# Kernel optimization log

Measured on AMD Instinct MI355X. Metric: run time of the kernel, lower is better.

Reference implementation:

```python
import jax, jax.numpy as jnp
import numpy as np


def setup_inputs() -> dict:
    key = jax.random.key(0)
    k1, k2 = jax.random.split(key)
    B, Fin, N = 8, 64, 4096
    Fout, K = 64, 20
    x = jax.random.normal(k1, (B, Fin, N), dtype=jnp.float32)
    W = jax.random.normal(k2, (Fout, 2 * Fin), dtype=jnp.float32) * (1.0 / np.sqrt(2 * Fin))
    b = jnp.zeros((Fout,), dtype=jnp.float32)
    return {"x": x, "W": W, "b": b, "k": K}


def reference(x, W, b, k):
    # x: [B, Fin, N]; W: [Fout, 2Fin] (1x1 conv weight); b: [Fout]
    B, Fin, N = x.shape
    xt = jnp.swapaxes(x, 1, 2)                      # [B, N, Fin]
    sq = jnp.sum(xt * xt, axis=2)                   # [B, N]
    # pairwise squared distances: ||xi||^2 - 2 xi.xj + ||xj||^2
    dist = -2.0 * jnp.einsum('bnf,bmf->bnm', xt, xt) + sq[:, :, None] + sq[:, None, :]
    # ascending sort, drop self (index 0), keep k nearest neighbors
    idx = jnp.argsort(dist, axis=2)[:, :, 1:k + 1]  # [B, N, k] int
    # gather neighbor features per batch
    nbr = jax.vmap(lambda pts, i: pts[i])(xt, idx)  # [B, N, k, Fin]
    central = xt[:, :, None, :]                     # [B, N, 1, Fin]
    ee = jnp.concatenate(
        [jnp.broadcast_to(central, (B, N, k, Fin)), nbr - central], axis=-1
    )                                               # [B, N, k, 2Fin]
    # 1x1 conv == dense over channel dim, then bias, then max over k
    h = jnp.einsum('bnkf,of->bnko', ee, W) + b      # [B, N, k, Fout]
    out = jnp.max(h, axis=2)                        # [B, N, Fout]
    return jnp.swapaxes(out, 1, 2)                  # [B, Fout, N]
```

## Files before the change

### kernel.cpp

```cpp
#include <hip/hip_runtime.h>
#include <hip/hip_bf16.h>
#include <float.h>


#define BB 8
#define FF 64
#define NN 4096
#define KK 20
#define CAP 64
#define SS 4
#define PAD 1.0f

typedef unsigned short ushort_t;
typedef unsigned long long u64;
typedef __attribute__((ext_vector_type(8))) _Float16 half8;
typedef __attribute__((ext_vector_type(4))) float floatx4;
typedef __attribute__((ext_vector_type(2))) float floatx2;
typedef __attribute__((ext_vector_type(2))) unsigned short ushortx2;
typedef __attribute__((ext_vector_type(4))) unsigned int uintx4;

__device__ __forceinline__ size_t plidx16(int b, int n, int k) {
  return ((size_t)b * 256 + (n >> 4)) * 1024 + (size_t)(k >> 3) * 128 + (size_t)(n & 15) * 8 + (k & 7);
}

__global__ void __launch_bounds__(256) prep_kernel(
    const float* __restrict__ x, const float* __restrict__ W,
    float* __restrict__ sq, float* __restrict__ Q,
    ushort_t* __restrict__ ph, ushort_t* __restrict__ pm)
{
  __shared__ float xs[64][65];
  __shared__ float w2[64][65];
  int t = threadIdx.x;
  int b = blockIdx.x >> 6;
  int n0 = (blockIdx.x & 63) << 6;
  const float* xb = x + (size_t)b * FF * NN;

  int nl = t & 63, fq = t >> 6;
  #pragma unroll
  for (int i = 0; i < 16; ++i) {
    int f = fq + i * 4;
    xs[f][nl] = xb[(size_t)f * NN + n0 + nl];
  }
  #pragma unroll
  for (int i = 0; i < 16; ++i) {
    int id = i * 256 + t;
    int o = id >> 6, f = id & 63;
    w2[o][f] = W[o * 128 + 64 + f];
  }
  __syncthreads();

  if (t < 64) {
    float s = 0.f;
    #pragma unroll
    for (int f = 0; f < FF; ++f) { float v = xs[f][t]; s += v * v; }
    sq[b * NN + n0 + t] = s;
  }
  int o = t & 63, g = t >> 6;
  for (int i = 0; i < 16; ++i) {
    int r = g + i * 4;
    int n = n0 + r;
    float acc = 0.f;
    #pragma unroll
    for (int f = 0; f < FF; ++f) acc += w2[o][f] * xs[f][r];
    Q[((size_t)b * NN + n) * FF + o] = acc;

    float v = xs[o][r] * 1.41421356237309515f;
    _Float16 hh = (_Float16)v;
    float hf = (float)hh;
    _Float16 mm = (_Float16)((v - hf) * 4096.0f);
    size_t pb = plidx16(b, n, o);
    ph[pb] = __builtin_bit_cast(unsigned short, hh);
    pm[pb] = __builtin_bit_cast(unsigned short, mm);
  }
}

__device__ __forceinline__ void bitonic32f(float& v0, float& v1, int l15)
{
  #pragma unroll
  for (int k = 2; k <= 32; k <<= 1) {
    #pragma unroll
    for (int j = k >> 1; j >= 1; j >>= 1) {
      bool dirup = ((2 * l15) & k) == 0;
      if (j >= 2) {
        int lj = j >> 1;
        float p0 = __shfl_xor(v0, lj, 16);
        float p1 = __shfl_xor(v1, lj, 16);
        bool lower = (l15 & lj) == 0;
        bool keepmin = (dirup == lower);
        v0 = keepmin ? fminf(v0, p0) : fmaxf(v0, p0);
        v1 = keepmin ? fminf(v1, p1) : fmaxf(v1, p1);
      } else {
        float lo = fminf(v0, v1), hi = fmaxf(v0, v1);
        v0 = dirup ? lo : hi;
        v1 = dirup ? hi : lo;
      }
    }
  }
}

__device__ __forceinline__ void bitonic64k(u64& v0, u64& v1, int l31)
{
  #pragma unroll
  for (int k = 2; k <= 64; k <<= 1) {
    #pragma unroll
    for (int j = k >> 1; j >= 1; j >>= 1) {
      bool dirup = ((2 * l31) & k) == 0;
      if (j >= 2) {
        int lj = j >> 1;
        u64 p0 = __shfl_xor(v0, lj, 32);
        u64 p1 = __shfl_xor(v1, lj, 32);
        bool lower = (l31 & lj) == 0;
        bool keepmin = (dirup == lower);
        u64 a0 = v0 < p0 ? v0 : p0, b0 = v0 < p0 ? p0 : v0;
        u64 a1 = v1 < p1 ? v1 : p1, b1 = v1 < p1 ? p1 : v1;
        v0 = keepmin ? a0 : b0;
        v1 = keepmin ? a1 : b1;
      } else {
        u64 lo = v0 < v1 ? v0 : v1, hi = v0 < v1 ? v1 : v0;
        v0 = dirup ? lo : hi;
        v1 = dirup ? hi : lo;
      }
    }
  }
}

__device__ __forceinline__ u64 mkkey(float d, unsigned short idx)
{
  unsigned ub = __float_as_uint(d);
  unsigned mono = ub ^ (0x80000000u | (unsigned)((int)ub >> 31));
  return ((u64)mono << 16) | idx;
}

__global__ void __launch_bounds__(256) knn_kernel(
    const ushort_t* __restrict__ ph, const ushort_t* __restrict__ pm,
    const float* __restrict__ sq, u64* __restrict__ keys2)
{
  __shared__ float    bufd[4][16][CAP];
  __shared__ ushort_t bufi[4][16][CAP];
  __shared__ int scnt[4][16];

  const int t = threadIdx.x;
  const int lane = t & 63;
  const int l15 = lane & 15;
  const int q = lane >> 4;
  const int wv = t >> 6;
  const int blk = blockIdx.x;
  const int slice = blk & 3;
  const int g = (blk >> 2) & 63;
  const int b = blk >> 8;
  const int n0w = (g * 4 + wv) * 16;

  const float* __restrict__ sqb = sq + (size_t)b * NN;
  const float MS = 2.44140625e-4f;
  const int laneoff = q * 128 + l15 * 8;

  const bool hasdiag = ((n0w >> 10) == slice);
  const int dmc = (n0w & 1023) >> 5;

  half8 Ah[2], Am[2];
  {
    size_t abase = ((size_t)b * 256 + (n0w >> 4)) * 1024 + laneoff;
    #pragma unroll
    for (int s = 0; s < 2; ++s) {
      Ah[s] = *(const half8*)(ph + abase + s * 512);
      Am[s] = *(const half8*)(pm + abase + s * 512);
      uintx4 uh = __builtin_bit_cast(uintx4, Ah[s]); uh ^= 0x80008000u;
      uintx4 um = __builtin_bit_cast(uintx4, Am[s]); um ^= 0x80008000u;
      Ah[s] = __builtin_bit_cast(half8, uh);
      Am[s] = __builtin_bit_cast(half8, um);
    }
  }

  float m1[4], m2[4];
  #pragma unroll
  for (int r = 0; r < 4; ++r) { m1[r] = FLT_MAX; m2[r] = FLT_MAX; }

  for (int mc = 0; mc < 32; ++mc) {
    const int m0 = slice * 1024 + mc * 32;
    size_t mbase = ((size_t)b * 256 + (m0 >> 4)) * 1024 + laneoff;
    float sv0 = sqb[m0 + l15];
    float sv1 = sqb[m0 + 16 + l15];
    floatx4 a1[2];
    #pragma unroll
    for (int e = 0; e < 4; ++e) { a1[0][e] = sv0; a1[1][e] = sv1; }
    #pragma unroll
    for (int ti = 0; ti < 2; ++ti) {
      #pragma unroll
      for (int s = 0; s < 2; ++s) {
        half8 Bh = *(const half8*)(ph + mbase + ti * 1024 + s * 512);
        a1[ti] = __builtin_amdgcn_mfma_f32_16x16x32_f16(Ah[s], Bh, a1[ti], 0, 0, 0);
      }
    }
    if (hasdiag && mc == dmc) {
      #pragma unroll
      for (int ti = 0; ti < 2; ++ti) {
        int mcol = m0 + 16 * ti + l15;
        #pragma unroll
        for (int r = 0; r < 4; ++r)
          if (mcol == n0w + 4 * q + r) a1[ti][r] = FLT_MAX;
      }
    }
    #pragma unroll
    for (int ti = 0; ti < 2; ++ti) {
      #pragma unroll
      for (int r = 0; r < 4; ++r) {
        float c = a1[ti][r];
        m2[r] = __builtin_amdgcn_fmed3f(c, m1[r], m2[r]);
        m1[r] = fminf(m1[r], c);
      }
    }
  }

  float taupad[4];
  #pragma unroll
  for (int r = 0; r < 4; ++r) {
    float v0 = m1[r], v1 = m2[r];
    bitonic32f(v0, v1, l15);
    taupad[r] = __shfl(v1, 9, 16) + PAD;
  }

  int cnt[4];
  #pragma unroll
  for (int r = 0; r < 4; ++r) cnt[r] = 0;

  for (int mc = 0; mc < 32; ++mc) {
    const int m0 = slice * 1024 + mc * 32;
    size_t mbase = ((size_t)b * 256 + (m0 >> 4)) * 1024 + laneoff;
    float sv0 = sqb[m0 + l15];
    float sv1 = sqb[m0 + 16 + l15];
    floatx4 a1[2], a2[2];
    #pragma unroll
    for (int e = 0; e < 4; ++e) {
      a1[0][e] = sv0; a1[1][e] = sv1;
      a2[0][e] = 0.f; a2[1][e] = 0.f;
    }
    #pragma unroll
    for (int ti = 0; ti < 2; ++ti) {
      #pragma unroll
      for (int s = 0; s < 2; ++s) {
        half8 Bh = *(const half8*)(ph + mbase + ti * 1024 + s * 512);
        half8 Bm = *(const half8*)(pm + mbase + ti * 1024 + s * 512);
        a1[ti] = __builtin_amdgcn_mfma_f32_16x16x32_f16(Ah[s], Bh, a1[ti], 0, 0, 0);
        a2[ti] = __builtin_amdgcn_mfma_f32_16x16x32_f16(Am[s], Bh, a2[ti], 0, 0, 0);
        a2[ti] = __builtin_amdgcn_mfma_f32_16x16x32_f16(Ah[s], Bm, a2[ti], 0, 0, 0);
      }
    }
    #pragma unroll
    for (int ti = 0; ti < 2; ++ti)
      #pragma unroll
      for (int r = 0; r < 4; ++r)
        a1[ti][r] = __builtin_fmaf(MS, a2[ti][r], a1[ti][r]);
    if (hasdiag && mc == dmc) {
      #pragma unroll
      for (int ti = 0; ti < 2; ++ti) {
        int mcol = m0 + 16 * ti + l15;
        #pragma unroll
        for (int r = 0; r < 4; ++r)
          if (mcol == n0w + 4 * q + r) a1[ti][r] = FLT_MAX;
      }
    }
    #pragma unroll
    for (int ti = 0; ti < 2; ++ti) {
      int mcol = m0 + 16 * ti + l15;
      #pragma unroll
      for (int r = 0; r < 4; ++r) {
        bool ok = a1[ti][r] <= taupad[r];
        unsigned long long bal = __ballot(ok);
        unsigned mh = (unsigned)((bal >> (q * 16)) & 0xFFFFull);
        int pre = __popc(mh & ((1u << l15) - 1u));
        int slot = cnt[r] + pre;
        if (ok && slot < CAP) {
          bufd[wv][4 * q + r][slot] = a1[ti][r];
          bufi[wv][4 * q + r][slot] = (ushort_t)mcol;
        }
        cnt[r] += __popc(mh);
      }
    }
  }

  if (l15 == 0) {
    #pragma unroll
    for (int r = 0; r < 4; ++r) scnt[wv][4 * q + r] = cnt[r];
  }
  __builtin_amdgcn_s_waitcnt(0);

  const int l31 = t & 31;
  const int hfw = (t >> 5) & 1;
  #pragma unroll
  for (int i = 0; i < 8; ++i) {
    int rloc = hfw * 8 + i;
    int c = scnt[wv][rloc];
    c = c < CAP ? c : CAP;
    floatx2  dv = *(const floatx2*)&bufd[wv][rloc][2 * l31];
    ushortx2 iv = *(const ushortx2*)&bufi[wv][rloc][2 * l31];
    u64 k0 = (2 * l31     < c) ? mkkey(dv[0], iv[0]) : ~0ull;
    u64 k1 = (2 * l31 + 1 < c) ? mkkey(dv[1], iv[1]) : ~0ull;
    bitonic64k(k0, k1, l31);
    u64 a = __shfl(k0, l31 >> 1, 32);
    u64 b2 = __shfl(k1, l31 >> 1, 32);
    u64 kv = (l31 & 1) ? b2 : a;
    if (l31 < KK) {
      size_t rowg = ((size_t)b * NN + n0w + rloc) * SS + slice;
      keys2[rowg * KK + l31] = kv;
    }
  }
}

__global__ void __launch_bounds__(256) merge_kernel(
    const u64* __restrict__ keys2, int* __restrict__ idxOut)
{
  int row = blockIdx.x * 256 + threadIdx.x;
  if (row >= BB * NN) return;
  u64 h[SS]; int p[SS];
  #pragma unroll
  for (int s = 0; s < SS; ++s) {
    p[s] = 0;
    h[s] = keys2[((size_t)row * SS + s) * KK];
  }
  int* op = idxOut + (size_t)row * KK;
  #pragma unroll
  for (int q = 0; q < KK; ++q) {
    int bs = 0;
    u64 bv = h[0];
    #pragma unroll
    for (int s = 1; s < SS; ++s) { if (h[s] < bv) { bv = h[s]; bs = s; } }
    op[q] = (int)(bv & 0xFFFFull);
    p[bs]++;
    h[bs] = (p[bs] < KK) ? keys2[((size_t)row * SS + bs) * KK + p[bs]] : ~0ull;
  }
}

__global__ void __launch_bounds__(256) gather_kernel(
    const float* __restrict__ x, const float* __restrict__ W,
    const float* __restrict__ bias,
    const float* __restrict__ Q, const int* __restrict__ idxIn,
    float* __restrict__ out)
{
  __shared__ float xs[64][65];
  __shared__ float wp[64][65];
  __shared__ float ot[64][65];
  __shared__ float bs[64];
  int t = threadIdx.x;
  int b = blockIdx.x >> 6;
  int n0 = (blockIdx.x & 63) << 6;
  const float* xb = x + (size_t)b * FF * NN;

  int nl0 = t & 63, fq = t >> 6;
  #pragma unroll
  for (int i = 0; i < 16; ++i) {
    int f = fq + i * 4;
    xs[f][nl0] = xb[(size_t)f * NN + n0 + nl0];
  }
  #pragma unroll
  for (int i = 0; i < 16; ++i) {
    int id = i * 256 + t;
    int o = id >> 6, f = id & 63;
    wp[o][f] = W[o * 128 + f] - W[o * 128 + 64 + f];
  }
  if (t < 64) bs[t] = bias[t];
  __syncthreads();

  int o = t & 63, g = t >> 6;
  for (int i = 0; i < 16; ++i) {
    int nl = g + i * 4;
    int n = n0 + nl;
    float p = bs[o];
    #pragma unroll
    for (int f = 0; f < FF; ++f) p += wp[o][f] * xs[f][nl];
    const int* ip = idxIn + ((size_t)b * NN + n) * KK;
    float m = -FLT_MAX;
    #pragma unroll
    for (int j = 0; j < KK; ++j) {
      int nb = ip[j];
      m = fmaxf(m, Q[((size_t)b * NN + nb) * FF + o]);
    }
    ot[nl][o] = p + m;
  }
  __syncthreads();
  for (int i = 0; i < 16; ++i) {
    int o2 = g + i * 4;
    int nl = t & 63;
    out[((size_t)b * FF + o2) * NN + n0 + nl] = ot[nl][o2];
  }
}

extern "C" void kernel_launch(void* const* d_in, const int* in_sizes, int n_in,
                              void* d_out, int out_size, void* d_ws, size_t ws_size,
                              hipStream_t stream)
{
  const float* x    = (const float*)d_in[0];
  const float* W    = (const float*)d_in[1];
  const float* bias = (const float*)d_in[2];
  float* out = (float*)d_out;

  int*   idxb = (int*)d_ws;
  float* sq   = (float*)(idxb + (size_t)BB * NN * KK);
  float* Q    = sq + (size_t)BB * NN;
  ushort_t* ph = (ushort_t*)(Q + (size_t)BB * NN * FF);
  ushort_t* pm = ph + (size_t)BB * NN * FF;
  u64*   keys2 = (u64*)(pm + (size_t)BB * NN * FF);

  prep_kernel<<<BB * (NN / 64), 256, 0, stream>>>(x, W, sq, Q, ph, pm);
  knn_kernel<<<BB * 64 * SS, 256, 0, stream>>>(ph, pm, sq, keys2);
  merge_kernel<<<(BB * NN + 255) / 256, 256, 0, stream>>>(keys2, idxb);
  gather_kernel<<<BB * (NN / 64), 256, 0, stream>>>(x, W, bias, Q, idxb, out);
}
```

Baseline: 280.3 us.

## Split kNN threshold pass into a separate kernel writing per-row tau to workspace

Result: slower. 286.0 us (+2.1%).

```diff
diff --git a/kernel.cpp b/kernel.cpp
--- a/kernel.cpp
+++ b/kernel.cpp
@@ -131,9 +131,95 @@
   return ((u64)mono << 16) | idx;
 }
 
-__global__ void __launch_bounds__(256) knn_kernel(
+__global__ void __launch_bounds__(256) knn_a_kernel(
+    const ushort_t* __restrict__ ph,
+    const float* __restrict__ sq, float* __restrict__ tauG)
+{
+  __shared__ float sqs[1024];
+
+  const int t = threadIdx.x;
+  const int lane = t & 63;
+  const int l15 = lane & 15;
+  const int q = lane >> 4;
+  const int blk = blockIdx.x;
+  const int slice = blk & 3;
+  const int g = (blk >> 2) & 63;
+  const int b = blk >> 8;
+  const int wv = t >> 6;
+  const int n0w = (g * 4 + wv) * 16;
+
+  const float* __restrict__ sqb = sq + (size_t)b * NN;
+  const int laneoff = q * 128 + l15 * 8;
+
+  #pragma unroll
+  for (int i = 0; i < 4; ++i)
+    sqs[t + i * 256] = sqb[slice * 1024 + t + i * 256];
+  __syncthreads();
+
+  const bool hasdiag = ((n0w >> 10) == slice);
+  const int dmc = (n0w & 1023) >> 5;
+
+  half8 Ah[2];
+  {
+    size_t abase = ((size_t)b * 256 + (n0w >> 4)) * 1024 + laneoff;
+    #pragma unroll
+    for (int s = 0; s < 2; ++s) {
+      Ah[s] = *(const half8*)(ph + abase + s * 512);
+      uintx4 uh = __builtin_bit_cast(uintx4, Ah[s]); uh ^= 0x80008000u;
+      Ah[s] = __builtin_bit_cast(half8, uh);
+    }
+  }
+
+  float m1[4], m2[4];
+  #pragma unroll
+  for (int r = 0; r < 4; ++r) { m1[r] = FLT_MAX; m2[r] = FLT_MAX; }
+
+  for (int mc = 0; mc < 32; ++mc) {
+    const int m0 = slice * 1024 + mc * 32;
+    size_t mbase = ((size_t)b * 256 + (m0 >> 4)) * 1024 + laneoff;
+    float sv0 = sqs[mc * 32 + l15];
+    float sv1 = sqs[mc * 32 + 16 + l15];
+    floatx4 a1[2];
+    #pragma unroll
+    for (int e = 0; e < 4; ++e) { a1[0][e] = sv0; a1[1][e] = sv1; }
+    #pragma unroll
+    for (int ti = 0; ti < 2; ++ti) {
+      #pragma unroll
+      for (int s = 0; s < 2; ++s) {
+        half8 Bh = *(const half8*)(ph + mbase + ti * 1024 + s * 512);
+        a1[ti] = __builtin_amdgcn_mfma_f32_16x16x32_f16(Ah[s], Bh, a1[ti], 0, 0, 0);
+      }
+    }
+    if (hasdiag && mc == dmc) {
+      #pragma unroll
+      for (int ti = 0; ti < 2; ++ti) {
+        int mcol = m0 + 16 * ti + l15;
+        #pragma unroll
+        for (int r = 0; r < 4; ++r)
+          if (mcol == n0w + 4 * q + r) a1[ti][r] = FLT_MAX;
+      }
+    }
+    #pragma unroll
+    for (int r = 0; r < 4; ++r) {
+      float c = fminf(a1[0][r], a1[1][r]);
+      m2[r] = __builtin_amdgcn_fmed3f(c, m1[r], m2[r]);
+      m1[r] = fminf(m1[r], c);
+    }
+  }
+
+  float* trow = tauG + ((size_t)(b * SS + slice)) * NN + n0w;
+  #pragma unroll
+  for (int r = 0; r < 4; ++r) {
+    float v0 = m1[r], v1 = m2[r];
+    bitonic32f(v0, v1, l15);
+    if (l15 == 9) trow[4 * q + r] = v1 + PAD;
+  }
+}
+
+__global__ void __launch_bounds__(256) knn_b_kernel(
     const ushort_t* __restrict__ ph, const ushort_t* __restrict__ pm,
-    const float* __restrict__ sq, u64* __restrict__ keys2)
+    const float* __restrict__ sq, const float* __restrict__ tauG,
+    u64* __restrict__ keys2)
 {
   __shared__ float    bufd[4][16][CAP];
   __shared__ ushort_t bufi[4][16][CAP];
@@ -171,53 +257,10 @@
     }
   }
 
-  float m1[4], m2[4];
-  #pragma unroll
-  for (int r = 0; r < 4; ++r) { m1[r] = FLT_MAX; m2[r] = FLT_MAX; }
-
-  for (int mc = 0; mc < 32; ++mc) {
-    const int m0 = slice * 1024 + mc * 32;
-    size_t mbase = ((size_t)b * 256 + (m0 >> 4)) * 1024 + laneoff;
-    float sv0 = sqb[m0 + l15];
-    float sv1 = sqb[m0 + 16 + l15];
-    floatx4 a1[2];
-    #pragma unroll
-    for (int e = 0; e < 4; ++e) { a1[0][e] = sv0; a1[1][e] = sv1; }
-    #pragma unroll
-    for (int ti = 0; ti < 2; ++ti) {
-      #pragma unroll
-      for (int s = 0; s < 2; ++s) {
-        half8 Bh = *(const half8*)(ph + mbase + ti * 1024 + s * 512);
-        a1[ti] = __builtin_amdgcn_mfma_f32_16x16x32_f16(Ah[s], Bh, a1[ti], 0, 0, 0);
-      }
-    }
-    if (hasdiag && mc == dmc) {
-      #pragma unroll
-      for (int ti = 0; ti < 2; ++ti) {
-        int mcol = m0 + 16 * ti + l15;
-        #pragma unroll
-        for (int r = 0; r < 4; ++r)
-          if (mcol == n0w + 4 * q + r) a1[ti][r] = FLT_MAX;
-      }
-    }
-    #pragma unroll
-    for (int ti = 0; ti < 2; ++ti) {
-      #pragma unroll
-      for (int r = 0; r < 4; ++r) {
-        float c = a1[ti][r];
-        m2[r] = __builtin_amdgcn_fmed3f(c, m1[r], m2[r]);
-        m1[r] = fminf(m1[r], c);
-      }
-    }
-  }
-
+  const float* trow = tauG + ((size_t)(b * SS + slice)) * NN + n0w;
   float taupad[4];
   #pragma unroll
-  for (int r = 0; r < 4; ++r) {
-    float v0 = m1[r], v1 = m2[r];
-    bitonic32f(v0, v1, l15);
-    taupad[r] = __shfl(v1, 9, 16) + PAD;
-  }
+  for (int r = 0; r < 4; ++r) taupad[r] = trow[4 * q + r];
 
   int cnt[4];
   #pragma unroll
@@ -399,9 +442,11 @@
   ushort_t* ph = (ushort_t*)(Q + (size_t)BB * NN * FF);
   ushort_t* pm = ph + (size_t)BB * NN * FF;
   u64*   keys2 = (u64*)(pm + (size_t)BB * NN * FF);
+  float* tauG = (float*)idxb;
 
   prep_kernel<<<BB * (NN / 64), 256, 0, stream>>>(x, W, sq, Q, ph, pm);
-  knn_kernel<<<BB * 64 * SS, 256, 0, stream>>>(ph, pm, sq, keys2);
+  knn_a_kernel<<<BB * 64 * SS, 256, 0, stream>>>(ph, sq, tauG);
+  knn_b_kernel<<<BB * 64 * SS, 256, 0, stream>>>(ph, pm, sq, tauG, keys2);
   merge_kernel<<<(BB * NN + 255) / 256, 256, 0, stream>>>(keys2, idxb);
   gather_kernel<<<BB * (NN / 64), 256, 0, stream>>>(x, W, bias, Q, idxb, out);
 }
```
